# Optimization experiments

Measured on AMD Instinct MI355X. Metric: run time of the kernel, lower is better.

Reference implementation:

```python
import jax, jax.numpy as jnp
import numpy as np
from jax import lax

N_NEURONS = 256
N_EDGES = 1024
BATCH = 128
HW = 28
KSIZE = 5
FC_HID = 200
N_CLS = 10


def _make_graph():
    # Replicates the torch __init__ random incidence construction; retries seeds
    # until the last neuron is reachable from neuron 0 (else torch forward loops forever).
    for seed in range(1000):
        rng = np.random.default_rng(seed)
        src = np.zeros(N_EDGES, np.int32)
        tgt = np.zeros(N_EDGES, np.int32)
        for e in range(N_EDGES):
            t = int(rng.choice(np.arange(1, N_NEURONS)))
            pool = np.arange(0, N_NEURONS - 1)
            if t < N_NEURONS - 1:
                pool = np.delete(pool, t)  # np.delete(range(0,N-1), target) as in source
            src[e] = int(rng.choice(pool))
            tgt[e] = t
        processed = np.zeros(N_NEURONS, bool)
        processed[0] = True
        frontier = [0]
        while frontier and not processed[-1]:
            nxt = set()
            for v in frontier:
                for m in tgt[src == v]:
                    if not processed[m]:
                        nxt.add(int(m))
            for m in nxt:
                processed[m] = True
            frontier = sorted(nxt)
        if processed[-1]:
            return src, tgt
    raise RuntimeError('no reachable graph found')


def _schedule(src, tgt, n):
    # Ordered input list per neuron (edge order, as np.where gives) + BFS waves from neuron 0.
    in_lists = [list(src[np.where(tgt == i)[0]]) for i in range(n)]
    waves = []
    processed = np.zeros(n, bool)
    frontier = [0]
    while True:
        waves.append(list(frontier))
        processed[frontier] = True
        if processed[n - 1]:
            break
        nxt = set()
        for v in frontier:
            for m in tgt[src == v]:
                if not processed[m]:
                    nxt.add(int(m))
        frontier = sorted(nxt)
        assert frontier, 'last neuron unreachable'
    return in_lists, waves


def setup_inputs() -> dict:
    src, tgt = _make_graph()
    rng = np.random.default_rng(123)
    deg = np.bincount(tgt, minlength=N_NEURONS)
    in_count = np.maximum(deg, 1)  # torch forces input_count>=1
    cmax = int(in_count.max())
    fan = np.sqrt(in_count.astype(np.float32) * KSIZE * KSIZE)
    conv_w = rng.normal(size=(N_NEURONS, 1, cmax, KSIZE, KSIZE)).astype(np.float32)
    conv_w /= fan[:, None, None, None, None]
    # zero out padding channels beyond each neuron's true in_count
    mask = (np.arange(cmax)[None, :] < in_count[:, None]).astype(np.float32)
    conv_w *= mask[:, None, :, None, None]
    conv_b = (0.01 * rng.normal(size=(N_NEURONS,))).astype(np.float32)
    deg_last = int(in_count[-1])
    fc1_w = (rng.normal(size=(FC_HID, deg_last * HW * HW)) / np.sqrt(deg_last * HW * HW)).astype(np.float32)
    fc1_b = np.zeros(FC_HID, np.float32)
    fc2_w = (rng.normal(size=(N_CLS, FC_HID)) / np.sqrt(FC_HID)).astype(np.float32)
    fc2_b = np.zeros(N_CLS, np.float32)
    x = jax.random.normal(jax.random.key(0), (BATCH, 1, HW, HW), jnp.float32)
    return {'x': x, 'src': jnp.asarray(src), 'tgt': jnp.asarray(tgt),
            'conv_w': jnp.asarray(conv_w), 'conv_b': jnp.asarray(conv_b),
            'fc1_w': jnp.asarray(fc1_w), 'fc1_b': jnp.asarray(fc1_b),
            'fc2_w': jnp.asarray(fc2_w), 'fc2_b': jnp.asarray(fc2_b)}


def _conv(g, w):  # g: [B,C,H,W], w: [1,C,5,5] -> [B,1,H,W], SAME padding 2
    return lax.conv_general_dilated(g, w, (1, 1), [(2, 2), (2, 2)])


def reference(x, src, tgt, conv_w, conv_b, fc1_w, fc1_b, fc2_w, fc2_b):
    src_np = np.asarray(src)
    tgt_np = np.asarray(tgt)
    n = int(conv_w.shape[0])
    cmax = int(conv_w.shape[2])
    B, H = x.shape[0], x.shape[2]
    in_lists, waves = _schedule(src_np, tgt_np, n)
    idx_pad = np.zeros((n, cmax), np.int32)  # pad idx 0 is safe: padded weight channels are zero
    for i, lst in enumerate(in_lists):
        idx_pad[i, :len(lst)] = lst

    out = jnp.zeros((n, B, H, H), x.dtype)  # per-neuron activations (unprocessed stay zero)
    hidden = None
    for wi, wave in enumerate(waves):
        snap = out  # within a wave, neurons read the previous wave's outputs
        if wi == 0:
            o0 = jax.nn.relu(_conv(x, conv_w[0, :, :1])[:, 0] + conv_b[0])
            out = out.at[0].set(o0)
            continue
        conv_nodes = [v for v in wave if v != n - 1]
        if conv_nodes:
            cn = jnp.asarray(np.array(conv_nodes, np.int32))
            g = snap[idx_pad[conv_nodes]]        # [K, Cmax, B, H, H]
            g = g.transpose(0, 2, 1, 3, 4)       # [K, B, Cmax, H, H]
            res = jax.vmap(_conv)(g, conv_w[cn])  # [K, B, 1, H, H]
            res = jax.nn.relu(res[:, :, 0] + conv_b[cn][:, None, None, None])
            out = out.at[cn].set(res)
        if (n - 1) in wave:
            lst = np.array(in_lists[n - 1], np.int32)
            comp = snap[lst].transpose(1, 0, 2, 3).reshape(B, -1)  # cat along channel then flatten
            hidden = jax.nn.relu(comp @ fc1_w.T + fc1_b)
    logits = hidden @ fc2_w.T + fc2_b
    return jax.nn.log_softmax(logits, axis=1)
```

## Files before the change

### kernel.cpp

```cpp
#include <hip/hip_runtime.h>

#define N_NEUR 256
#define N_EDGE 1024
#define BATCH  128
#define HWDIM  28
#define IMG    784
#define FCH    200
#define NCLS   10
#define INF_W  0x3fffffff
#define SLOTS  257
#define XSLOT  256
#define TSZ    1024
#define NT1    1024
#define NWAVE  16
#define FCCH   8

#define ACT_FLOATS ((size_t)BATCH * SLOTS * TSZ)

__global__ __launch_bounds__(NT1, 4)
void conv_kernel(const float* __restrict__ x, const int* __restrict__ src,
                 const int* __restrict__ tgt, const float* __restrict__ conv_w,
                 const float* __restrict__ conv_b, float* __restrict__ act,
                 int* __restrict__ gsched, int cmax)
{
    const int tid = threadIdx.x;
    const int b   = blockIdx.x;

    __shared__ float s_tiles[NWAVE][2][TSZ];
    __shared__ int   s_off[N_NEUR + 2];
    __shared__ int   s_dat[N_EDGE];
    __shared__ int   s_wn[N_NEUR];
    __shared__ int   s_wo[N_NEUR + 2];
    __shared__ int   s_na[N_NEUR];
    __shared__ int   s_W;
    __shared__ int   s_done;

    int* e_src = (int*)&s_tiles[0][0][0];
    int* e_tgt = e_src + N_EDGE;
    int* wv    = e_tgt + N_EDGE;

    if (tid < N_EDGE) { e_src[tid] = src[tid]; e_tgt[tid] = tgt[tid]; }
    if (tid < N_NEUR) wv[tid] = (tid == 0) ? 0 : INF_W;
    __syncthreads();
    for (int w = 0; w < N_NEUR; ++w) {
        if (tid == 0) s_done = (wv[N_NEUR - 1] != INF_W);
        __syncthreads();
        if (s_done) break;
        {
            int s = e_src[tid], t = e_tgt[tid];
            if (wv[s] == w && wv[t] == INF_W) wv[t] = w + 1;
        }
        __syncthreads();
    }
    if (tid < N_NEUR) {
        int na = 0;
        const int wvv = wv[tid];
        for (int e = 0; e < N_EDGE; ++e)
            if (e_tgt[e] == tid && wv[e_src[e]] < wvv) ++na;
        if (tid == 0) na = 1;
        s_na[tid] = na;
    }
    __syncthreads();
    if (tid == 0) {
        int o = 0;
        for (int v = 0; v < N_NEUR; ++v) { s_off[v] = o; o += s_na[v]; }
        s_off[N_NEUR] = o;
        s_W = wv[N_NEUR - 1];
    }
    __syncthreads();
    if (tid < N_NEUR) {
        if (tid == 0) {
            s_dat[s_off[0]] = XSLOT;
        } else {
            int o = s_off[tid], c = 0;
            const int wvv = wv[tid];
            for (int e = 0; e < N_EDGE; ++e) {
                if (e_tgt[e] == tid) {
                    if (wv[e_src[e]] < wvv) s_dat[o++] = e_src[e] | (c << 9);
                    ++c;
                }
            }
        }
    }
    __syncthreads();
    {
        const int Wl = s_W;
        if (tid <= Wl + 1) {
            int cn = 0;
            for (int v2 = 0; v2 < N_NEUR - 1; ++v2) if (wv[v2] < tid) ++cn;
            s_wo[tid] = cn;
        }
        if (tid < N_NEUR - 1 && wv[tid] <= Wl) {
            int pos = 0; const int mw = wv[tid];
            for (int v2 = 0; v2 < N_NEUR - 1; ++v2) {
                int w2 = wv[v2];
                if (w2 < mw || (w2 == mw && v2 < tid)) ++pos;
            }
            s_wn[pos] = tid;
        }
    }
    __syncthreads();
    {
        const int naL = s_off[N_NEUR] - s_off[N_NEUR - 1];
        if (tid == 0) gsched[0] = naL;
        if (tid < naL) gsched[1 + tid] = s_dat[s_off[N_NEUR - 1] + tid];
    }
    for (int u = tid; u < SLOTS * 72; u += NT1) {
        const int t = u % 72, tile = u / 72;
        float* tp = act + (((size_t)b * SLOTS + tile) << 10);
        if (t < 16) {
            int eb = (t < 8) ? t * 8 : 960 + (t - 8) * 8;
            float4 z = make_float4(0.f, 0.f, 0.f, 0.f);
            ((float4*)(tp + eb))[0] = z; ((float4*)(tp + eb))[1] = z;
        } else {
            int s = t - 16;
            int eb = (2 + (s >> 1)) * 32 + ((s & 1) ? 30 : 0);
            *((float2*)(tp + eb)) = make_float2(0.f, 0.f);
        }
    }
    for (int u = tid; u < 196; u += NT1) {
        const int row = u / 7, col = (u - row * 7) * 4;
        float4 v4 = *(const float4*)(x + b * IMG + row * HWDIM + col);
        float* tp = act + (((size_t)b * SLOTS + XSLOT) << 10) + (row + 2) * 32 + col + 2;
        *(float2*)tp       = make_float2(v4.x, v4.y);
        *(float2*)(tp + 2) = make_float2(v4.z, v4.w);
    }
    __syncthreads();

    const int wid  = tid >> 6;
    const int lane = tid & 63;
    const bool la  = lane < 49;
    const int cy   = lane / 7, cx = lane - 7 * (lane / 7);
    float* buf0 = &s_tiles[wid][0][0];
    float* buf1 = &s_tiles[wid][1][0];

    for (int w = 0; w <= s_W; ++w) {
        for (int ni = s_wo[w] + wid; ni < s_wo[w + 1]; ni += NWAVE) {
            const int v  = __builtin_amdgcn_readfirstlane(s_wn[ni]);
            const int o0 = s_off[v], o1 = s_off[v + 1];
            const float bias = conv_b[v];
            float acc[16];
            #pragma unroll
            for (int k = 0; k < 16; ++k) acc[k] = bias;

            float4 stg[4];
            {
                const int u0 = s_dat[o0] & 511;
                const float4* gs = (const float4*)(act + (((size_t)b * SLOTS + u0) << 10));
                #pragma unroll
                for (int i = 0; i < 4; ++i) stg[i] = gs[lane + 64 * i];
            }
            for (int o = o0; o < o1; ++o) {
                const int pk = __builtin_amdgcn_readfirstlane(s_dat[o]);
                const int c  = pk >> 9;
                float* buf = (o & 1) ? buf1 : buf0;
                #pragma unroll
                for (int i = 0; i < 4; ++i) {
                    const int fi  = lane + 64 * i;
                    const int row = fi >> 3, cg = fi & 7;
                    ((float4*)buf)[(row << 3) | (cg ^ ((row >> 2) & 7))] = stg[i];
                }
                if (o + 1 < o1) {
                    const int un = s_dat[o + 1] & 511;
                    const float4* gs = (const float4*)(act + (((size_t)b * SLOTS + un) << 10));
                    #pragma unroll
                    for (int i = 0; i < 4; ++i) stg[i] = gs[lane + 64 * i];
                }
                const float* wp = conv_w + ((size_t)v * cmax + c) * 25;
                float wg[25];
                #pragma unroll
                for (int k = 0; k < 25; ++k) wg[k] = wp[k];
                if (la) {
                    #pragma unroll
                    for (int r = 0; r < 8; ++r) {
                        const int row = 4 * cy + r;
                        const int sw  = (row >> 2) & 7;
                        float4 fa = ((const float4*)buf)[(row << 3) | (cx ^ sw)];
                        float4 fb = ((const float4*)buf)[(row << 3) | ((cx + 1) ^ sw)];
                        const float f[8] = {fa.x, fa.y, fa.z, fa.w, fb.x, fb.y, fb.z, fb.w};
                        #pragma unroll
                        for (int i = 0; i < 4; ++i) {
                            const int tr = r - i;
                            if (tr < 0 || tr > 4) continue;
                            #pragma unroll
                            for (int dx = 0; dx < 5; ++dx) {
                                const float wvv = wg[tr * 5 + dx];
                                #pragma unroll
                                for (int j = 0; j < 4; ++j)
                                    acc[i * 4 + j] = fmaf(f[j + dx], wvv, acc[i * 4 + j]);
                            }
                        }
                    }
                }
            }
            if (la) {
                float* gd = act + (((size_t)b * SLOTS + v) << 10);
                #pragma unroll
                for (int i = 0; i < 4; ++i) {
                    float* p = gd + (2 + 4 * cy + i) * 32 + 2 + 4 * cx;
                    *(float2*)p       = make_float2(fmaxf(acc[i*4+0], 0.f), fmaxf(acc[i*4+1], 0.f));
                    *(float2*)(p + 2) = make_float2(fmaxf(acc[i*4+2], 0.f), fmaxf(acc[i*4+3], 0.f));
                }
            }
        }
        __syncthreads();
    }
}

__global__ __launch_bounds__(512, 2)
void fc1_kernel(const float* __restrict__ act, const float* __restrict__ fc1_w,
                const float* __restrict__ fc1_b, float* __restrict__ hidden,
                const int* __restrict__ gsched, int dlast)
{
    const int tid = threadIdx.x;
    const int b   = blockIdx.x;
    __shared__ float s_comp[FCCH][IMG];
    const int naL  = gsched[0];
    const int h    = tid >> 1, half = tid & 1;
    float acc = 0.f;
    for (int cb = 0; cb < naL; cb += FCCH) {
        const int nc = (naL - cb < FCCH) ? (naL - cb) : FCCH;
        __syncthreads();
        for (int idx = tid; idx < nc * IMG; idx += 512) {
            const int a = idx / IMG, px = idx - a * IMG;
            const int u = gsched[1 + cb + a] & 511;
            const int row = px / HWDIM, col = px - row * HWDIM;
            s_comp[a][px] = act[(((size_t)b * SLOTS + u) << 10) + (row + 2) * 32 + col + 2];
        }
        __syncthreads();
        if (h < FCH) {
            for (int a = 0; a < nc; ++a) {
                const int k = gsched[1 + cb + a] >> 9;
                const float4* w4 = (const float4*)(fc1_w + (size_t)h * ((size_t)dlast * IMG)
                                                   + (size_t)k * IMG + half * 392);
                const float4* c4 = (const float4*)(&s_comp[a][half * 392]);
                #pragma unroll 7
                for (int j = 0; j < 98; ++j) {
                    const float4 wv4 = w4[j], cv4 = c4[j];
                    acc = fmaf(cv4.x, wv4.x, acc);
                    acc = fmaf(cv4.y, wv4.y, acc);
                    acc = fmaf(cv4.z, wv4.z, acc);
                    acc = fmaf(cv4.w, wv4.w, acc);
                }
            }
        }
    }
    acc += __shfl_xor(acc, 1);
    if (h < FCH && half == 0) hidden[b * FCH + h] = fmaxf(acc + fc1_b[h], 0.f);
}

__global__ __launch_bounds__(128, 1)
void fc2_kernel(const float* __restrict__ hidden, const float* __restrict__ fc2_w,
                const float* __restrict__ fc2_b, float* __restrict__ dout)
{
    const int b = threadIdx.x;
    float hr[FCH];
    const float* hp = hidden + b * FCH;
    for (int h = 0; h < FCH; h += 2) {
        float2 v2 = *(const float2*)(hp + h);
        hr[h] = v2.x; hr[h + 1] = v2.y;
    }
    float lg[NCLS], m = -1e30f;
    #pragma unroll
    for (int c = 0; c < NCLS; ++c) {
        float a2 = fc2_b[c];
        const float* wr = fc2_w + c * FCH;
        for (int h = 0; h < FCH; ++h) a2 = fmaf(hr[h], wr[h], a2);
        lg[c] = a2;
        m = fmaxf(m, a2);
    }
    float s = 0.0f;
    #pragma unroll
    for (int c = 0; c < NCLS; ++c) s += expf(lg[c] - m);
    const float ls = m + logf(s);
    #pragma unroll
    for (int c = 0; c < NCLS; ++c) dout[b * NCLS + c] = lg[c] - ls;
}

extern "C" void kernel_launch(void* const* d_in, const int* in_sizes, int n_in,
                              void* d_out, int out_size, void* d_ws, size_t ws_size,
                              hipStream_t stream) {
    const float* x      = (const float*)d_in[0];
    const int*   src    = (const int*)d_in[1];
    const int*   tgt    = (const int*)d_in[2];
    const float* conv_w = (const float*)d_in[3];
    const float* conv_b = (const float*)d_in[4];
    const float* fc1_w  = (const float*)d_in[5];
    const float* fc1_b  = (const float*)d_in[6];
    const float* fc2_w  = (const float*)d_in[7];
    const float* fc2_b  = (const float*)d_in[8];
    float* out = (float*)d_out;
    float* ws  = (float*)d_ws;

    const int cmax  = in_sizes[3] / (N_NEUR * 25);
    const int dlast = in_sizes[5] / (FCH * IMG);

    float* act    = ws;
    float* hidden = ws + ACT_FLOATS;
    int*   gsched = (int*)(hidden + BATCH * FCH);

    hipLaunchKernelGGL(conv_kernel, dim3(BATCH), dim3(NT1), 0, stream,
                       x, src, tgt, conv_w, conv_b, act, gsched, cmax);
    hipLaunchKernelGGL(fc1_kernel, dim3(BATCH), dim3(512), 0, stream,
                       act, fc1_w, fc1_b, hidden, gsched, dlast);
    hipLaunchKernelGGL(fc2_kernel, dim3(1), dim3(128), 0, stream,
                       hidden, fc2_w, fc2_b, out);
}
```

Measured before the change: 321.0 us.

## Split conv neurons across two wavefronts by row halves and retile fc1 over batch

The conv stage now assigns each neuron to two wavefronts, each computing half of the output rows (14 rows) from an 18-row halo tile. This doubles the parallelism per wave and shrinks LDS use. The per-input loop now double-buffers both activation tiles and weights with a two-deep prefetch. fc1 is restructured into a batch-tile × hidden-tile grid so that each weight row is reused across 16 batch elements staged in LDS, replacing per-sample blocks that reread the full weight matrix. The cost is duplicated halo loads and possibly idle wavefronts when a wave has few neurons.

```diff
diff --git a/kernel.cpp b/kernel.cpp
--- a/kernel.cpp
+++ b/kernel.cpp
@@ -13,7 +13,7 @@
 #define TSZ    1024
 #define NT1    1024
 #define NWAVE  16
-#define FCCH   8
+#define HROWS  18
 
 #define ACT_FLOATS ((size_t)BATCH * SLOTS * TSZ)
 
@@ -26,7 +26,7 @@
     const int tid = threadIdx.x;
     const int b   = blockIdx.x;
 
-    __shared__ float s_tiles[NWAVE][2][TSZ];
+    __shared__ float s_half[NWAVE][2][HROWS * 32];
     __shared__ int   s_off[N_NEUR + 2];
     __shared__ int   s_dat[N_EDGE];
     __shared__ int   s_wn[N_NEUR];
@@ -35,7 +35,7 @@
     __shared__ int   s_W;
     __shared__ int   s_done;
 
-    int* e_src = (int*)&s_tiles[0][0][0];
+    int* e_src = (int*)&s_half[0][0][0];
     int* e_tgt = e_src + N_EDGE;
     int* wv    = e_tgt + N_EDGE;
 
@@ -129,75 +129,111 @@
 
     const int wid  = tid >> 6;
     const int lane = tid & 63;
+    const int half = wid & 1;
+    const int rs   = half * 14;
     const bool la  = lane < 49;
     const int cy   = lane / 7, cx = lane - 7 * (lane / 7);
-    float* buf0 = &s_tiles[wid][0][0];
-    float* buf1 = &s_tiles[wid][1][0];
+    float* bufA = &s_half[wid][0][0];
+    float* bufB = &s_half[wid][1][0];
+
+    auto loadStg = [&](float4* st, int oo) {
+        const int uu = __builtin_amdgcn_readfirstlane(s_dat[oo]) & 511;
+        const float4* gs = (const float4*)(act + (((size_t)b * SLOTS + uu) << 10)) + rs * 8;
+        st[0] = gs[lane];
+        st[1] = gs[lane + 64];
+        if (lane < 16) st[2] = gs[lane + 128];
+    };
+    auto storeLds = [&](float* buf, const float4* st) {
+        float4* b4 = (float4*)buf;
+        {
+            const int fl = lane, lr = fl >> 3, cg = fl & 7;
+            b4[(lr << 3) | (cg ^ ((lr >> 2) & 7))] = st[0];
+        }
+        {
+            const int fl = lane + 64, lr = fl >> 3, cg = fl & 7;
+            b4[(lr << 3) | (cg ^ ((lr >> 2) & 7))] = st[1];
+        }
+        if (lane < 16) {
+            const int fl = lane + 128, lr = fl >> 3, cg = fl & 7;
+            b4[(lr << 3) | (cg ^ ((lr >> 2) & 7))] = st[2];
+        }
+    };
 
     for (int w = 0; w <= s_W; ++w) {
-        for (int ni = s_wo[w] + wid; ni < s_wo[w + 1]; ni += NWAVE) {
+        for (int ni2 = 2 * s_wo[w] + wid; ni2 < 2 * s_wo[w + 1]; ni2 += NWAVE) {
+            const int ni = ni2 >> 1;
             const int v  = __builtin_amdgcn_readfirstlane(s_wn[ni]);
             const int o0 = s_off[v], o1 = s_off[v + 1];
             const float bias = conv_b[v];
-            float acc[16];
+            float acc[8];
             #pragma unroll
-            for (int k = 0; k < 16; ++k) acc[k] = bias;
-
-            float4 stg[4];
+            for (int k = 0; k < 8; ++k) acc[k] = bias;
+
+            float4 stgA[3], stgB[3];
+            float  wgA[25], wgB[25];
+            loadStg(stgA, o0);
+            if (o0 + 1 < o1) loadStg(stgB, o0 + 1);
             {
-                const int u0 = s_dat[o0] & 511;
-                const float4* gs = (const float4*)(act + (((size_t)b * SLOTS + u0) << 10));
+                const int pk = __builtin_amdgcn_readfirstlane(s_dat[o0]);
+                const float* wp = conv_w + ((size_t)v * cmax + (pk >> 9)) * 25;
                 #pragma unroll
-                for (int i = 0; i < 4; ++i) stg[i] = gs[lane + 64 * i];
-            }
-            for (int o = o0; o < o1; ++o) {
-                const int pk = __builtin_amdgcn_readfirstlane(s_dat[o]);
-                const int c  = pk >> 9;
-                float* buf = (o & 1) ? buf1 : buf0;
+                for (int k = 0; k < 25; ++k) wgA[k] = wp[k];
+            }
+
+            auto computeBuf = [&](const float* buf, const float* wg) {
+                if (!la) return;
+                const float4* b4 = (const float4*)buf;
                 #pragma unroll
-                for (int i = 0; i < 4; ++i) {
-                    const int fi  = lane + 64 * i;
-                    const int row = fi >> 3, cg = fi & 7;
-                    ((float4*)buf)[(row << 3) | (cg ^ ((row >> 2) & 7))] = stg[i];
-                }
-                if (o + 1 < o1) {
-                    const int un = s_dat[o + 1] & 511;
-                    const float4* gs = (const float4*)(act + (((size_t)b * SLOTS + un) << 10));
+                for (int r = 0; r < 6; ++r) {
+                    const int lr = 2 * cy + r;
+                    const int sw = (lr >> 2) & 7;
+                    float4 fa = b4[(lr << 3) | (cx ^ sw)];
+                    float4 fb = b4[(lr << 3) | ((cx + 1) ^ sw)];
+                    const float f[8] = {fa.x, fa.y, fa.z, fa.w, fb.x, fb.y, fb.z, fb.w};
                     #pragma unroll
-                    for (int i = 0; i < 4; ++i) stg[i] = gs[lane + 64 * i];
-                }
-                const float* wp = conv_w + ((size_t)v * cmax + c) * 25;
-                float wg[25];
-                #pragma unroll
-                for (int k = 0; k < 25; ++k) wg[k] = wp[k];
-                if (la) {
-                    #pragma unroll
-                    for (int r = 0; r < 8; ++r) {
-                        const int row = 4 * cy + r;
-                        const int sw  = (row >> 2) & 7;
-                        float4 fa = ((const float4*)buf)[(row << 3) | (cx ^ sw)];
-                        float4 fb = ((const float4*)buf)[(row << 3) | ((cx + 1) ^ sw)];
-                        const float f[8] = {fa.x, fa.y, fa.z, fa.w, fb.x, fb.y, fb.z, fb.w};
+                    for (int i = 0; i < 2; ++i) {
+                        const int tr = r - i;
+                        if (tr < 0 || tr > 4) continue;
                         #pragma unroll
-                        for (int i = 0; i < 4; ++i) {
-                            const int tr = r - i;
-                            if (tr < 0 || tr > 4) continue;
+                        for (int dx = 0; dx < 5; ++dx) {
+                            const float wvv = wg[tr * 5 + dx];
                             #pragma unroll
-                            for (int dx = 0; dx < 5; ++dx) {
-                                const float wvv = wg[tr * 5 + dx];
-                                #pragma unroll
-                                for (int j = 0; j < 4; ++j)
-                                    acc[i * 4 + j] = fmaf(f[j + dx], wvv, acc[i * 4 + j]);
-                            }
+                            for (int j = 0; j < 4; ++j)
+                                acc[i * 4 + j] = fmaf(f[j + dx], wvv, acc[i * 4 + j]);
                         }
                     }
                 }
-            }
+            };
+
+            int o = o0;
+            while (true) {
+                storeLds(bufA, stgA);
+                if (o + 2 < o1) loadStg(stgA, o + 2);
+                if (o + 1 < o1) {
+                    const int pk = __builtin_amdgcn_readfirstlane(s_dat[o + 1]);
+                    const float* wp = conv_w + ((size_t)v * cmax + (pk >> 9)) * 25;
+                    #pragma unroll
+                    for (int k = 0; k < 25; ++k) wgB[k] = wp[k];
+                }
+                computeBuf(bufA, wgA);
+                ++o; if (o >= o1) break;
+                storeLds(bufB, stgB);
+                if (o + 2 < o1) loadStg(stgB, o + 2);
+                if (o + 1 < o1) {
+                    const int pk = __builtin_amdgcn_readfirstlane(s_dat[o + 1]);
+                    const float* wp = conv_w + ((size_t)v * cmax + (pk >> 9)) * 25;
+                    #pragma unroll
+                    for (int k = 0; k < 25; ++k) wgA[k] = wp[k];
+                }
+                computeBuf(bufB, wgB);
+                ++o; if (o >= o1) break;
+            }
+
             if (la) {
                 float* gd = act + (((size_t)b * SLOTS + v) << 10);
                 #pragma unroll
-                for (int i = 0; i < 4; ++i) {
-                    float* p = gd + (2 + 4 * cy + i) * 32 + 2 + 4 * cx;
+                for (int i = 0; i < 2; ++i) {
+                    float* p = gd + (rs + 2 + 2 * cy + i) * 32 + 2 + 4 * cx;
                     *(float2*)p       = make_float2(fmaxf(acc[i*4+0], 0.f), fmaxf(acc[i*4+1], 0.f));
                     *(float2*)(p + 2) = make_float2(fmaxf(acc[i*4+2], 0.f), fmaxf(acc[i*4+3], 0.f));
                 }
@@ -207,46 +243,56 @@
     }
 }
 
-__global__ __launch_bounds__(512, 2)
+#define FC1_BT 16
+#define FC1_HT 16
+#define FC1_STRIDE 900
+
+__global__ __launch_bounds__(256, 2)
 void fc1_kernel(const float* __restrict__ act, const float* __restrict__ fc1_w,
                 const float* __restrict__ fc1_b, float* __restrict__ hidden,
                 const int* __restrict__ gsched, int dlast)
 {
     const int tid = threadIdx.x;
-    const int b   = blockIdx.x;
-    __shared__ float s_comp[FCCH][IMG];
-    const int naL  = gsched[0];
-    const int h    = tid >> 1, half = tid & 1;
+    const int bt  = blockIdx.x & 7;
+    const int ht  = blockIdx.x >> 3;
+    const int b0  = bt * FC1_BT;
+    const int h0  = ht * FC1_HT;
+    __shared__ float s_act[FC1_BT * FC1_STRIDE];
+    const int naL = gsched[0];
+    const int bb  = tid & 15, hh = tid >> 4;
+    const int h   = h0 + hh;
     float acc = 0.f;
-    for (int cb = 0; cb < naL; cb += FCCH) {
-        const int nc = (naL - cb < FCCH) ? (naL - cb) : FCCH;
-        __syncthreads();
-        for (int idx = tid; idx < nc * IMG; idx += 512) {
-            const int a = idx / IMG, px = idx - a * IMG;
-            const int u = gsched[1 + cb + a] & 511;
-            const int row = px / HWDIM, col = px - row * HWDIM;
-            s_comp[a][px] = act[(((size_t)b * SLOTS + u) << 10) + (row + 2) * 32 + col + 2];
+
+    for (int a = 0; a < naL; ++a) {
+        const int pk = gsched[1 + a];
+        const int u = pk & 511, k = pk >> 9;
+        __syncthreads();
+        for (int idx = tid; idx < FC1_BT * 224; idx += 256) {
+            const int bi = idx / 224, rr = idx - bi * 224;
+            const int r = rr >> 3, cg = rr & 7;
+            const float4 vv = *((const float4*)(act +
+                (((size_t)(b0 + bi) * SLOTS + u) << 10) + (r + 2) * 32) + cg);
+            *(float4*)(&s_act[bi * FC1_STRIDE + r * 32 + cg * 4]) = vv;
         }
         __syncthreads();
         if (h < FCH) {
-            for (int a = 0; a < nc; ++a) {
-                const int k = gsched[1 + cb + a] >> 9;
-                const float4* w4 = (const float4*)(fc1_w + (size_t)h * ((size_t)dlast * IMG)
-                                                   + (size_t)k * IMG + half * 392);
-                const float4* c4 = (const float4*)(&s_comp[a][half * 392]);
-                #pragma unroll 7
-                for (int j = 0; j < 98; ++j) {
-                    const float4 wv4 = w4[j], cv4 = c4[j];
-                    acc = fmaf(cv4.x, wv4.x, acc);
-                    acc = fmaf(cv4.y, wv4.y, acc);
-                    acc = fmaf(cv4.z, wv4.z, acc);
-                    acc = fmaf(cv4.w, wv4.w, acc);
-                }
-            }
-        }
-    }
-    acc += __shfl_xor(acc, 1);
-    if (h < FCH && half == 0) hidden[b * FCH + h] = fmaxf(acc + fc1_b[h], 0.f);
+            const float* wrow = fc1_w + (size_t)h * ((size_t)dlast * IMG) + (size_t)k * IMG;
+            const float* Tb   = &s_act[bb * FC1_STRIDE];
+            for (int r = 0; r < HWDIM; ++r) {
+                const float4* w4 = (const float4*)(wrow + r * HWDIM);
+                const float*  tr = Tb + r * 32 + 2;
+                #pragma unroll
+                for (int q = 0; q < 7; ++q) {
+                    const float4 wv = w4[q];
+                    acc = fmaf(tr[4*q+0], wv.x, acc);
+                    acc = fmaf(tr[4*q+1], wv.y, acc);
+                    acc = fmaf(tr[4*q+2], wv.z, acc);
+                    acc = fmaf(tr[4*q+3], wv.w, acc);
+                }
+            }
+        }
+    }
+    if (h < FCH) hidden[(b0 + bb) * FCH + h] = fmaxf(acc + fc1_b[h], 0.f);
 }
 
 __global__ __launch_bounds__(128, 1)
@@ -265,7 +311,7 @@
     for (int c = 0; c < NCLS; ++c) {
         float a2 = fc2_b[c];
         const float* wr = fc2_w + c * FCH;
-        for (int h = 0; h < FCH; ++h) a2 = fmaf(hr[h], wr[h], a2);
+        for (int hh = 0; hh < FCH; ++hh) a2 = fmaf(hr[hh], wr[hh], a2);
         lg[c] = a2;
         m = fmaxf(m, a2);
     }
@@ -301,7 +347,7 @@
 
     hipLaunchKernelGGL(conv_kernel, dim3(BATCH), dim3(NT1), 0, stream,
                        x, src, tgt, conv_w, conv_b, act, gsched, cmax);
-    hipLaunchKernelGGL(fc1_kernel, dim3(BATCH), dim3(512), 0, stream,
+    hipLaunchKernelGGL(fc1_kernel, dim3(104), dim3(256), 0, stream,
                        act, fc1_w, fc1_b, hidden, gsched, dlast);
     hipLaunchKernelGGL(fc2_kernel, dim3(1), dim3(128), 0, stream,
                        hidden, fc2_w, fc2_b, out);
```

Result: no change. 327.2 us (+2.0%).
